# Performance work log

Measured on AMD Instinct MI355X. Metric: run time of the kernel, lower is better.

## Reference

```python
import jax, jax.numpy as jnp
import numpy as np

N = 50000      # nodes
E = 800000     # edges (before self-loops)
C_IN = 128
HID = 128
C_OUT = 64
B = 64         # graphs in batch
NEG_SLOPE = 0.2
EPS = 1e-16


def setup_inputs() -> dict:
    key = jax.random.key(0)
    ks = jax.random.split(key, 12)
    x = jax.random.normal(ks[0], (N, C_IN), dtype=jnp.float32)
    edge_index = jax.random.randint(ks[1], (2, E), 0, N, dtype=jnp.int64)
    batch = jnp.sort(jax.random.randint(ks[2], (N,), 0, B, dtype=jnp.int64))
    g1 = 1.0 / np.sqrt(C_IN)
    g2 = 1.0 / np.sqrt(HID)
    return {
        'x': x,
        'edge_index': edge_index,
        'batch': batch,
        'W1': jax.random.normal(ks[3], (C_IN, HID), jnp.float32) * g1,
        'a_src1': jax.random.normal(ks[4], (HID,), jnp.float32) * g2,
        'a_dst1': jax.random.normal(ks[5], (HID,), jnp.float32) * g2,
        'b1': jnp.zeros((HID,), jnp.float32),
        'W2': jax.random.normal(ks[6], (HID, C_OUT), jnp.float32) * g2,
        'a_src2': jax.random.normal(ks[7], (C_OUT,), jnp.float32) / np.sqrt(C_OUT),
        'a_dst2': jax.random.normal(ks[8], (C_OUT,), jnp.float32) / np.sqrt(C_OUT),
        'b2': jnp.zeros((C_OUT,), jnp.float32),
    }


def _gat_conv(x, src, dst, W, a_src, a_dst, b):
    # PyG GATConv, heads=1, self-loops already appended to (src, dst).
    h = x @ W                                   # [N, F]
    alpha = h[src] @ a_src + h[dst] @ a_dst     # [E'] per-edge logit
    alpha = jax.nn.leaky_relu(alpha, NEG_SLOPE)
    # segment softmax over incoming edges of each destination node
    amax = jax.ops.segment_max(alpha, dst, num_segments=N)
    e = jnp.exp(alpha - amax[dst])
    denom = jax.ops.segment_sum(e, dst, num_segments=N)
    att = e / (denom[dst] + EPS)                # [E']
    out = jax.ops.segment_sum(att[:, None] * h[src], dst, num_segments=N)
    return out + b


def reference(x, edge_index, batch, W1, a_src1, a_dst1, b1, W2, a_src2, a_dst2, b2):
    loop = jnp.arange(N, dtype=edge_index.dtype)
    src = jnp.concatenate([edge_index[0], loop])  # add_self_loops=True
    dst = jnp.concatenate([edge_index[1], loop])
    h = _gat_conv(x, src, dst, W1, a_src1, a_dst1, b1)
    h = jax.nn.relu(h)
    h = _gat_conv(h, src, dst, W2, a_src2, a_dst2, b2)
    # global mean pool over graph ids
    sums = jax.ops.segment_sum(h, batch, num_segments=B)          # [B, C_OUT]
    cnt = jax.ops.segment_sum(jnp.ones((N,), h.dtype), batch, num_segments=B)
    pooled = sums / jnp.maximum(cnt, 1.0)[:, None]
    return jax.nn.log_softmax(pooled, axis=1)
```

## Files before the change

kernel.cpp:

```cpp
#include <hip/hip_runtime.h>
#include <math.h>

#define NN 50000
#define EE 800000
#define EP (EE + NN)
#define COUT 64
#define BB 64
#define NEG_SLOPE 0.2f
#define EPSF 1e-16f
#define NPART 8
#define PNODES (NN / NPART)
#define CAPE 128
#define GM 782

typedef unsigned short u16;
typedef __attribute__((ext_vector_type(8))) short bf16x8;
typedef __attribute__((ext_vector_type(4))) float f32x4;

__device__ __forceinline__ u16 f2b(float f) {
    union { float f; unsigned u; } v; v.f = f;
    unsigned u = v.u;
    return (u16)((u + 0x7FFFu + ((u >> 16) & 1u)) >> 16);
}
__device__ __forceinline__ float b2f(u16 h) {
    union { unsigned u; float f; } v; v.u = ((unsigned)h) << 16;
    return v.f;
}
__device__ __forceinline__ float leaky(float v) {
    return (v > 0.f) ? v : NEG_SLOPE * v;
}

__global__ __launch_bounds__(256) void k_pre(const float* __restrict__ W1,
                                             const float* __restrict__ W2,
                                             u16* __restrict__ W1t,
                                             u16* __restrict__ W2t,
                                             int* __restrict__ deg,
                                             float* __restrict__ sums) {
    int b = blockIdx.x;
    if (b < 96) {
        int t = b * 256 + threadIdx.x;
        if (t < 128 * 128) {
            int c = t >> 7, k = t & 127;
            W1t[t] = f2b(W1[k * 128 + c]);
        } else {
            int o = t - 128 * 128;
            int c = o >> 7, k = o & 127;
            W2t[o] = f2b(W2[k * 64 + c]);
        }
    } else {
        int n = (b - 96) * 256 + threadIdx.x;
        if (n < NN) deg[n] = 0;
        if (n < BB * COUT) sums[n] = 0.f;
    }
}

__global__ __launch_bounds__(256) void k_scatter(const int* __restrict__ src,
                                                 const int* __restrict__ dst,
                                                 int* __restrict__ deg,
                                                 int* __restrict__ col_ell) {
    int v = blockIdx.x & (NPART - 1);
    int cid = blockIdx.x >> 3;
    int nchunk = gridDim.x >> 3;
    int lo = v * PNODES, hi = lo + PNODES;
    for (int e = cid * 256 + threadIdx.x; e < EP; e += nchunk * 256) {
        int dd = (e < EE) ? dst[e] : (e - EE);
        if (dd >= lo && dd < hi) {
            int s = (e < EE) ? src[e] : dd;
            int pos = atomicAdd(&deg[dd], 1);
            if (pos < CAPE) col_ell[(size_t)dd * CAPE + pos] = s;
        }
    }
}

template <int F, bool ABF16>
__device__ __forceinline__ void gemm_body(int bx,
                                          const void* __restrict__ Xv,
                                          const u16* __restrict__ Wt,
                                          u16* __restrict__ H,
                                          const float* __restrict__ a_src,
                                          const float* __restrict__ a_dst,
                                          float* __restrict__ sdot,
                                          float* __restrict__ ddot) {
    __shared__ u16 Ab[64 * 128];
    __shared__ u16 Bb[F * 128];
    int tid = threadIdx.x;
    int row0 = bx * 64;

    if (ABF16) {
        const u16* X = (const u16*)Xv;
        #pragma unroll
        for (int it = 0; it < 4; it++) {
            int c = it * 256 + tid;
            int row = c >> 4;
            int k8 = (c & 15) * 8;
            int grow = row0 + row;
            uint4 val = {0u, 0u, 0u, 0u};
            if (grow < NN) val = *(const uint4*)&X[(size_t)grow * 128 + k8];
            *(uint4*)&Ab[row * 128 + (k8 ^ ((row & 7) << 3))] = val;
        }
    } else {
        const float* X = (const float*)Xv;
        #pragma unroll
        for (int it = 0; it < 8; it++) {
            int c = it * 256 + tid;
            int e = c * 4;
            int row = e >> 7;
            int col = e & 127;
            int grow = row0 + row;
            float4 v = {0.f, 0.f, 0.f, 0.f};
            if (grow < NN) v = *(const float4*)&X[(size_t)grow * 128 + col];
            ushort4 o;
            o.x = f2b(v.x); o.y = f2b(v.y); o.z = f2b(v.z); o.w = f2b(v.w);
            *(ushort4*)&Ab[row * 128 + (col ^ ((row & 7) << 3))] = o;
        }
    }
    const int NB = F * 128 / 8 / 256;
    #pragma unroll
    for (int it = 0; it < NB; it++) {
        int c = it * 256 + tid;
        int col = c >> 4;
        int k8 = (c & 15) * 8;
        uint4 val = *(const uint4*)&Wt[col * 128 + k8];
        *(uint4*)&Bb[col * 128 + (k8 ^ ((col & 7) << 3))] = val;
    }
    __syncthreads();

    int w = tid >> 6, l = tid & 63;
    int g = l >> 4;
    int rA = l & 15;
    const int NT = F / 16;
    f32x4 acc[NT];
    #pragma unroll
    for (int ct = 0; ct < NT; ct++) {
        acc[ct][0] = 0.f; acc[ct][1] = 0.f; acc[ct][2] = 0.f; acc[ct][3] = 0.f;
    }
    int arow = w * 16 + rA;
    int abase = arow * 128;
    int sw = (rA & 7) << 3;
    #pragma unroll
    for (int ks = 0; ks < 4; ks++) {
        int koff = ks * 32 + g * 8;
        bf16x8 af = *(const bf16x8*)&Ab[abase + (koff ^ sw)];
        #pragma unroll
        for (int ct = 0; ct < NT; ct++) {
            int bcol = ct * 16 + rA;
            bf16x8 bfv = *(const bf16x8*)&Bb[bcol * 128 + (koff ^ sw)];
            acc[ct] = __builtin_amdgcn_mfma_f32_16x16x32_bf16(af, bfv, acc[ct], 0, 0, 0);
        }
    }

    float asv[NT], adv[NT];
    #pragma unroll
    for (int ct = 0; ct < NT; ct++) {
        asv[ct] = a_src[ct * 16 + rA];
        adv[ct] = a_dst[ct * 16 + rA];
    }
    float ps[4] = {0.f, 0.f, 0.f, 0.f};
    float pd[4] = {0.f, 0.f, 0.f, 0.f};
    #pragma unroll
    for (int ct = 0; ct < NT; ct++) {
        #pragma unroll
        for (int r = 0; r < 4; r++) {
            ps[r] += acc[ct][r] * asv[ct];
            pd[r] += acc[ct][r] * adv[ct];
        }
    }
    #pragma unroll
    for (int r = 0; r < 4; r++) {
        int grow = row0 + w * 16 + g * 4 + r;
        if (grow < NN) {
            #pragma unroll
            for (int ct = 0; ct < NT; ct++) {
                H[(size_t)grow * F + ct * 16 + rA] = f2b(acc[ct][r]);
            }
        }
    }
    #pragma unroll
    for (int r = 0; r < 4; r++) {
        #pragma unroll
        for (int off = 1; off < 16; off <<= 1) {
            ps[r] += __shfl_xor(ps[r], off);
            pd[r] += __shfl_xor(pd[r], off);
        }
    }
    if (rA == 0) {
        #pragma unroll
        for (int r = 0; r < 4; r++) {
            int grow = row0 + w * 16 + g * 4 + r;
            if (grow < NN) { sdot[grow] = ps[r]; ddot[grow] = pd[r]; }
        }
    }
}

__global__ __launch_bounds__(256) void k_gemm1(const float* __restrict__ x,
                                               const u16* __restrict__ W1t,
                                               u16* __restrict__ h1,
                                               const float* __restrict__ as1,
                                               const float* __restrict__ ad1,
                                               float* __restrict__ s1,
                                               float* __restrict__ d1) {
    gemm_body<128, false>(blockIdx.x, x, W1t, h1, as1, ad1, s1, d1);
}

__global__ __launch_bounds__(256) void k_gemm2(const u16* __restrict__ x2,
                                               const u16* __restrict__ W2t,
                                               u16* __restrict__ h2,
                                               const float* __restrict__ as2,
                                               const float* __restrict__ ad2,
                                               float* __restrict__ s2,
                                               float* __restrict__ d2) {
    gemm_body<64, true>(blockIdx.x, x2, W2t, h2, as2, ad2, s2, d2);
}

template <int ROWB>
__device__ __forceinline__ float stage_weights(const int* __restrict__ colrow,
                                               const float* __restrict__ s,
                                               float dn, int deg, int lane,
                                               float* __restrict__ wl,
                                               int* __restrict__ wc) {
    float M = -INFINITY;
    for (int e0 = 0; e0 < deg; e0 += 64) {
        int e = e0 + lane;
        float l = -INFINITY; int c = 0;
        if (e < deg) { c = colrow[e]; l = leaky(s[c] + dn); }
        wl[e0 + lane] = l;
        wc[e0 + lane] = c * ROWB;
        float cm = l;
        #pragma unroll
        for (int off = 32; off; off >>= 1) cm = fmaxf(cm, __shfl_xor(cm, off));
        M = fmaxf(M, cm);
    }
    float Sl = 0.f;
    for (int i0 = 0; i0 < deg; i0 += 64) {
        float u = __expf(wl[i0 + lane] - M);
        wl[i0 + lane] = u;
        Sl += u;
    }
    #pragma unroll
    for (int off = 32; off; off >>= 1) Sl += __shfl_xor(Sl, off);
    return 1.f / (Sl + EPSF);
}

__global__ __launch_bounds__(256) void k_fused1(const int* __restrict__ degv,
                                                const int* __restrict__ col_ell,
                                                const float* __restrict__ s,
                                                const float* __restrict__ d,
                                                const u16* __restrict__ H,
                                                const float* __restrict__ bias,
                                                u16* __restrict__ outb) {
    const int F = 128;
    __shared__ float wl[4][CAPE];
    __shared__ int   wc[4][CAPE];
    int w = threadIdx.x >> 6;
    int lane = threadIdx.x & 63;
    int n = blockIdx.x * 4 + w;
    int deg = degv[n];
    if (deg > CAPE) deg = CAPE;
    const int* colrow = col_ell + (size_t)n * CAPE;
    float dn = d[n];
    const char* Hb = (const char*)H + lane * 4;
    float2 acc = {0.f, 0.f};

    float invS = stage_weights<F * 2>(colrow, s, dn, deg, lane, wl[w], wc[w]);
    int i = 0;
    for (; i + 8 <= deg; i += 8) {
        float u0 = wl[w][i+0], u1 = wl[w][i+1], u2 = wl[w][i+2], u3 = wl[w][i+3];
        float u4 = wl[w][i+4], u5 = wl[w][i+5], u6 = wl[w][i+6], u7 = wl[w][i+7];
        int o0 = wc[w][i+0], o1 = wc[w][i+1], o2 = wc[w][i+2], o3 = wc[w][i+3];
        int o4 = wc[w][i+4], o5 = wc[w][i+5], o6 = wc[w][i+6], o7 = wc[w][i+7];
        ushort2 r0 = *(const ushort2*)(Hb + o0);
        ushort2 r1 = *(const ushort2*)(Hb + o1);
        ushort2 r2 = *(const ushort2*)(Hb + o2);
        ushort2 r3 = *(const ushort2*)(Hb + o3);
        ushort2 r4 = *(const ushort2*)(Hb + o4);
        ushort2 r5 = *(const ushort2*)(Hb + o5);
        ushort2 r6 = *(const ushort2*)(Hb + o6);
        ushort2 r7 = *(const ushort2*)(Hb + o7);
        acc.x += u0 * b2f(r0.x); acc.y += u0 * b2f(r0.y);
        acc.x += u1 * b2f(r1.x); acc.y += u1 * b2f(r1.y);
        acc.x += u2 * b2f(r2.x); acc.y += u2 * b2f(r2.y);
        acc.x += u3 * b2f(r3.x); acc.y += u3 * b2f(r3.y);
        acc.x += u4 * b2f(r4.x); acc.y += u4 * b2f(r4.y);
        acc.x += u5 * b2f(r5.x); acc.y += u5 * b2f(r5.y);
        acc.x += u6 * b2f(r6.x); acc.y += u6 * b2f(r6.y);
        acc.x += u7 * b2f(r7.x); acc.y += u7 * b2f(r7.y);
    }
    for (; i < deg; ++i) {
        float u = wl[w][i];
        ushort2 r = *(const ushort2*)(Hb + wc[w][i]);
        acc.x += u * b2f(r.x); acc.y += u * b2f(r.y);
    }
    float2 b = *(const float2*)&bias[lane * 2];
    acc.x = fmaxf(acc.x * invS + b.x, 0.f);
    acc.y = fmaxf(acc.y * invS + b.y, 0.f);
    ushort2 o; o.x = f2b(acc.x); o.y = f2b(acc.y);
    *(ushort2*)&outb[(size_t)n * F + lane * 2] = o;
}

#define NPW 4
__global__ __launch_bounds__(256) void k_fused2(const int* __restrict__ degv,
                                                const int* __restrict__ col_ell,
                                                const float* __restrict__ s,
                                                const float* __restrict__ d,
                                                const u16* __restrict__ H,
                                                const float* __restrict__ bias,
                                                const int* __restrict__ batch,
                                                float* __restrict__ sums) {
    const int F = 64;
    __shared__ float wl[4][CAPE];
    __shared__ int   wc[4][CAPE];
    int wave = threadIdx.x >> 6;
    int lane = threadIdx.x & 63;
    int base = (blockIdx.x * 4 + wave) * NPW;
    int lim = base + NPW;
    float bs = bias[lane];
    const char* Hb = (const char*)H + lane * 2;
    float gacc = 0.f;
    int gb = batch[base];

    for (int n = base; n < lim; ++n) {
        int b = batch[n];
        if (b != gb) {
            atomicAdd(&sums[gb * COUT + lane], gacc);
            gacc = 0.f; gb = b;
        }
        int deg = degv[n];
        if (deg > CAPE) deg = CAPE;
        const int* colrow = col_ell + (size_t)n * CAPE;
        float dn = d[n];
        float acc = 0.f;

        float invS = stage_weights<F * 2>(colrow, s, dn, deg, lane, wl[wave], wc[wave]);
        int i = 0;
        for (; i + 8 <= deg; i += 8) {
            float u0 = wl[wave][i+0], u1 = wl[wave][i+1], u2 = wl[wave][i+2], u3 = wl[wave][i+3];
            float u4 = wl[wave][i+4], u5 = wl[wave][i+5], u6 = wl[wave][i+6], u7 = wl[wave][i+7];
            int o0 = wc[wave][i+0], o1 = wc[wave][i+1], o2 = wc[wave][i+2], o3 = wc[wave][i+3];
            int o4 = wc[wave][i+4], o5 = wc[wave][i+5], o6 = wc[wave][i+6], o7 = wc[wave][i+7];
            u16 r0 = *(const u16*)(Hb + o0); u16 r1 = *(const u16*)(Hb + o1);
            u16 r2 = *(const u16*)(Hb + o2); u16 r3 = *(const u16*)(Hb + o3);
            u16 r4 = *(const u16*)(Hb + o4); u16 r5 = *(const u16*)(Hb + o5);
            u16 r6 = *(const u16*)(Hb + o6); u16 r7 = *(const u16*)(Hb + o7);
            acc += u0 * b2f(r0) + u1 * b2f(r1) + u2 * b2f(r2) + u3 * b2f(r3);
            acc += u4 * b2f(r4) + u5 * b2f(r5) + u6 * b2f(r6) + u7 * b2f(r7);
        }
        for (; i < deg; ++i) {
            acc += wl[wave][i] * b2f(*(const u16*)(Hb + wc[wave][i]));
        }
        gacc += acc * invS + bs;
    }
    atomicAdd(&sums[gb * COUT + lane], gacc);
}

__global__ __launch_bounds__(256) void k_logsm(const float* __restrict__ sums,
                                               const int* __restrict__ batch,
                                               float* __restrict__ out) {
    int wave = threadIdx.x >> 6;
    int lane = threadIdx.x & 63;
    int g = blockIdx.x * 4 + wave;
    if (g >= BB) return;
    int lo = 0, hi = NN;
    while (lo < hi) { int mid = (lo + hi) >> 1; if (batch[mid] < g) lo = mid + 1; else hi = mid; }
    int l2 = lo, h2 = NN;
    while (l2 < h2) { int mid = (l2 + h2) >> 1; if (batch[mid] < g + 1) l2 = mid + 1; else h2 = mid; }
    float cnt = (float)(h2 - lo);
    float mean = sums[g * COUT + lane] / fmaxf(cnt, 1.f);
    float mx = mean;
    #pragma unroll
    for (int off = 32; off; off >>= 1) mx = fmaxf(mx, __shfl_xor(mx, off));
    float ex = __expf(mean - mx);
    float sm = ex;
    #pragma unroll
    for (int off = 32; off; off >>= 1) sm += __shfl_xor(sm, off);
    out[g * COUT + lane] = mean - mx - logf(sm);
}

extern "C" void kernel_launch(void* const* d_in, const int* in_sizes, int n_in,
                              void* d_out, int out_size, void* d_ws, size_t ws_size,
                              hipStream_t stream) {
    const float* x      = (const float*)d_in[0];
    const int*   eidx   = (const int*)d_in[1];
    const int*   batch  = (const int*)d_in[2];
    const float* W1     = (const float*)d_in[3];
    const float* a_src1 = (const float*)d_in[4];
    const float* a_dst1 = (const float*)d_in[5];
    const float* b1     = (const float*)d_in[6];
    const float* W2     = (const float*)d_in[7];
    const float* a_src2 = (const float*)d_in[8];
    const float* a_dst2 = (const float*)d_in[9];
    const float* b2     = (const float*)d_in[10];
    float* out = (float*)d_out;

    const int* src = eidx;
    const int* dst = eidx + EE;

    char* w = (char*)d_ws;
    auto alloc = [&](size_t bytes) { void* p = (void*)w; w += (bytes + 255) & ~(size_t)255; return p; };
    float* sums  = (float*)alloc((size_t)BB * COUT * 4);
    float* s1    = (float*)alloc((size_t)NN * 4);
    float* d1    = (float*)alloc((size_t)NN * 4);
    float* s2    = (float*)alloc((size_t)NN * 4);
    float* d2    = (float*)alloc((size_t)NN * 4);
    int* deg     = (int*)alloc((size_t)NN * 4);
    int* col_ell = (int*)alloc((size_t)NN * CAPE * 4);
    u16* h1      = (u16*)alloc((size_t)NN * 128 * 2);
    u16* x2      = (u16*)alloc((size_t)NN * 128 * 2);
    u16* h2      = (u16*)alloc((size_t)NN * 64 * 2);
    u16* W1t     = (u16*)alloc((size_t)128 * 128 * 2);
    u16* W2t     = (u16*)alloc((size_t)64 * 128 * 2);

    dim3 blk(256);
    int gN4 = (NN + 3) / 4;

    k_pre<<<292, blk, 0, stream>>>(W1, W2, W1t, W2t, deg, sums);
    k_scatter<<<2048, blk, 0, stream>>>(src, dst, deg, col_ell);

    k_gemm1<<<GM, blk, 0, stream>>>(x, W1t, h1, a_src1, a_dst1, s1, d1);
    k_fused1<<<gN4, blk, 0, stream>>>(deg, col_ell, s1, d1, h1, b1, x2);

    k_gemm2<<<GM, blk, 0, stream>>>(x2, W2t, h2, a_src2, a_dst2, s2, d2);
    k_fused2<<<NN / (4 * NPW), blk, 0, stream>>>(deg, col_ell, s2, d2, h2, b2, batch, sums);

    k_logsm<<<(BB + 3) / 4, blk, 0, stream>>>(sums, batch, out);
}
```

Before: 151.0 us.

## Vectorize neighbor gathers across lane groups and vectorize edge scatter loads

Both aggregation kernels now split each wave into four lane groups, each handling a different neighbor. Each lane loads 16 bytes (layer 1) or 8 bytes (layer 2) of bf16 features per neighbor instead of 2 or 4 bytes, and partial sums are combined with cross-group shuffles. The edge scatter kernel reads destination indices as int4 and handles self-loops in a separate loop, which removes the per-edge branch. The aggregation loop rounds the degree up to a multiple of 8, so it relies on the staged weight and offset arrays holding zero weights and valid offsets in the padded slots. It also adds shuffle-reduction work and leaves only one lane group doing the writes.

```diff
diff --git a/kernel.cpp b/kernel.cpp
--- a/kernel.cpp
+++ b/kernel.cpp
@@ -25,6 +25,12 @@
 __device__ __forceinline__ float b2f(u16 h) {
     union { unsigned u; float f; } v; v.u = ((unsigned)h) << 16;
     return v.f;
+}
+__device__ __forceinline__ float lo16(unsigned v) {
+    union { unsigned u; float f; } x; x.u = v << 16; return x.f;
+}
+__device__ __forceinline__ float hi16(unsigned v) {
+    union { unsigned u; float f; } x; x.u = v & 0xffff0000u; return x.f;
 }
 __device__ __forceinline__ float leaky(float v) {
     return (v > 0.f) ? v : NEG_SLOPE * v;
@@ -62,13 +68,29 @@
     int cid = blockIdx.x >> 3;
     int nchunk = gridDim.x >> 3;
     int lo = v * PNODES, hi = lo + PNODES;
-    for (int e = cid * 256 + threadIdx.x; e < EP; e += nchunk * 256) {
-        int dd = (e < EE) ? dst[e] : (e - EE);
-        if (dd >= lo && dd < hi) {
-            int s = (e < EE) ? src[e] : dd;
-            int pos = atomicAdd(&deg[dd], 1);
-            if (pos < CAPE) col_ell[(size_t)dd * CAPE + pos] = s;
-        }
+    for (int q = cid * 256 + threadIdx.x; q < EE / 4; q += nchunk * 256) {
+        int4 d4 = *(const int4*)&dst[q * 4];
+        int e = q * 4;
+        if (d4.x >= lo && d4.x < hi) {
+            int pos = atomicAdd(&deg[d4.x], 1);
+            if (pos < CAPE) col_ell[(size_t)d4.x * CAPE + pos] = src[e];
+        }
+        if (d4.y >= lo && d4.y < hi) {
+            int pos = atomicAdd(&deg[d4.y], 1);
+            if (pos < CAPE) col_ell[(size_t)d4.y * CAPE + pos] = src[e + 1];
+        }
+        if (d4.z >= lo && d4.z < hi) {
+            int pos = atomicAdd(&deg[d4.z], 1);
+            if (pos < CAPE) col_ell[(size_t)d4.z * CAPE + pos] = src[e + 2];
+        }
+        if (d4.w >= lo && d4.w < hi) {
+            int pos = atomicAdd(&deg[d4.w], 1);
+            if (pos < CAPE) col_ell[(size_t)d4.w * CAPE + pos] = src[e + 3];
+        }
+    }
+    for (int n = lo + cid * 256 + threadIdx.x; n < hi; n += nchunk * 256) {
+        int pos = atomicAdd(&deg[n], 1);
+        if (pos < CAPE) col_ell[(size_t)n * CAPE + pos] = n;
     }
 }
 
@@ -258,43 +280,44 @@
     if (deg > CAPE) deg = CAPE;
     const int* colrow = col_ell + (size_t)n * CAPE;
     float dn = d[n];
-    const char* Hb = (const char*)H + lane * 4;
-    float2 acc = {0.f, 0.f};
 
     float invS = stage_weights<F * 2>(colrow, s, dn, deg, lane, wl[w], wc[w]);
-    int i = 0;
-    for (; i + 8 <= deg; i += 8) {
-        float u0 = wl[w][i+0], u1 = wl[w][i+1], u2 = wl[w][i+2], u3 = wl[w][i+3];
-        float u4 = wl[w][i+4], u5 = wl[w][i+5], u6 = wl[w][i+6], u7 = wl[w][i+7];
-        int o0 = wc[w][i+0], o1 = wc[w][i+1], o2 = wc[w][i+2], o3 = wc[w][i+3];
-        int o4 = wc[w][i+4], o5 = wc[w][i+5], o6 = wc[w][i+6], o7 = wc[w][i+7];
-        ushort2 r0 = *(const ushort2*)(Hb + o0);
-        ushort2 r1 = *(const ushort2*)(Hb + o1);
-        ushort2 r2 = *(const ushort2*)(Hb + o2);
-        ushort2 r3 = *(const ushort2*)(Hb + o3);
-        ushort2 r4 = *(const ushort2*)(Hb + o4);
-        ushort2 r5 = *(const ushort2*)(Hb + o5);
-        ushort2 r6 = *(const ushort2*)(Hb + o6);
-        ushort2 r7 = *(const ushort2*)(Hb + o7);
-        acc.x += u0 * b2f(r0.x); acc.y += u0 * b2f(r0.y);
-        acc.x += u1 * b2f(r1.x); acc.y += u1 * b2f(r1.y);
-        acc.x += u2 * b2f(r2.x); acc.y += u2 * b2f(r2.y);
-        acc.x += u3 * b2f(r3.x); acc.y += u3 * b2f(r3.y);
-        acc.x += u4 * b2f(r4.x); acc.y += u4 * b2f(r4.y);
-        acc.x += u5 * b2f(r5.x); acc.y += u5 * b2f(r5.y);
-        acc.x += u6 * b2f(r6.x); acc.y += u6 * b2f(r6.y);
-        acc.x += u7 * b2f(r7.x); acc.y += u7 * b2f(r7.y);
-    }
-    for (; i < deg; ++i) {
-        float u = wl[w][i];
-        ushort2 r = *(const ushort2*)(Hb + wc[w][i]);
-        acc.x += u * b2f(r.x); acc.y += u * b2f(r.y);
-    }
-    float2 b = *(const float2*)&bias[lane * 2];
-    acc.x = fmaxf(acc.x * invS + b.x, 0.f);
-    acc.y = fmaxf(acc.y * invS + b.y, 0.f);
-    ushort2 o; o.x = f2b(acc.x); o.y = f2b(acc.y);
-    *(ushort2*)&outb[(size_t)n * F + lane * 2] = o;
+
+    int g = lane >> 4;
+    int sub = lane & 15;
+    const char* Hb = (const char*)H + sub * 16;
+    float acc[8] = {0.f, 0.f, 0.f, 0.f, 0.f, 0.f, 0.f, 0.f};
+    int degR = (deg + 7) & ~7;
+    for (int i = 0; i < degR; i += 8) {
+        float u0 = wl[w][i + g];
+        int   o0 = wc[w][i + g];
+        float u1 = wl[w][i + 4 + g];
+        int   o1 = wc[w][i + 4 + g];
+        uint4 p0 = *(const uint4*)(Hb + o0);
+        uint4 p1 = *(const uint4*)(Hb + o1);
+        acc[0] += u0 * lo16(p0.x); acc[1] += u0 * hi16(p0.x);
+        acc[2] += u0 * lo16(p0.y); acc[3] += u0 * hi16(p0.y);
+        acc[4] += u0 * lo16(p0.z); acc[5] += u0 * hi16(p0.z);
+        acc[6] += u0 * lo16(p0.w); acc[7] += u0 * hi16(p0.w);
+        acc[0] += u1 * lo16(p1.x); acc[1] += u1 * hi16(p1.x);
+        acc[2] += u1 * lo16(p1.y); acc[3] += u1 * hi16(p1.y);
+        acc[4] += u1 * lo16(p1.z); acc[5] += u1 * hi16(p1.z);
+        acc[6] += u1 * lo16(p1.w); acc[7] += u1 * hi16(p1.w);
+    }
+    #pragma unroll
+    for (int j = 0; j < 8; j++) {
+        acc[j] += __shfl_xor(acc[j], 16);
+        acc[j] += __shfl_xor(acc[j], 32);
+    }
+    if (g == 0) {
+        ushort o8[8];
+        #pragma unroll
+        for (int j = 0; j < 8; j++) {
+            float v = fmaxf(acc[j] * invS + bias[sub * 8 + j], 0.f);
+            o8[j] = f2b(v);
+        }
+        *(uint4*)&outb[(size_t)n * F + sub * 8] = *(const uint4*)o8;
+    }
 }
 
 #define NPW 4
@@ -311,45 +334,62 @@
     __shared__ int   wc[4][CAPE];
     int wave = threadIdx.x >> 6;
     int lane = threadIdx.x & 63;
+    int g = lane >> 4;
+    int sub = lane & 15;
     int base = (blockIdx.x * 4 + wave) * NPW;
     int lim = base + NPW;
-    float bs = bias[lane];
-    const char* Hb = (const char*)H + lane * 2;
-    float gacc = 0.f;
+    float bs[4];
+    #pragma unroll
+    for (int j = 0; j < 4; j++) bs[j] = bias[sub * 4 + j];
+    const char* Hb = (const char*)H + sub * 8;
+    float gacc[4] = {0.f, 0.f, 0.f, 0.f};
     int gb = batch[base];
 
     for (int n = base; n < lim; ++n) {
         int b = batch[n];
         if (b != gb) {
-            atomicAdd(&sums[gb * COUT + lane], gacc);
-            gacc = 0.f; gb = b;
+            if (g == 0) {
+                #pragma unroll
+                for (int j = 0; j < 4; j++)
+                    atomicAdd(&sums[gb * COUT + sub * 4 + j], gacc[j]);
+            }
+            #pragma unroll
+            for (int j = 0; j < 4; j++) gacc[j] = 0.f;
+            gb = b;
         }
         int deg = degv[n];
         if (deg > CAPE) deg = CAPE;
         const int* colrow = col_ell + (size_t)n * CAPE;
         float dn = d[n];
-        float acc = 0.f;
 
         float invS = stage_weights<F * 2>(colrow, s, dn, deg, lane, wl[wave], wc[wave]);
-        int i = 0;
-        for (; i + 8 <= deg; i += 8) {
-            float u0 = wl[wave][i+0], u1 = wl[wave][i+1], u2 = wl[wave][i+2], u3 = wl[wave][i+3];
-            float u4 = wl[wave][i+4], u5 = wl[wave][i+5], u6 = wl[wave][i+6], u7 = wl[wave][i+7];
-            int o0 = wc[wave][i+0], o1 = wc[wave][i+1], o2 = wc[wave][i+2], o3 = wc[wave][i+3];
-            int o4 = wc[wave][i+4], o5 = wc[wave][i+5], o6 = wc[wave][i+6], o7 = wc[wave][i+7];
-            u16 r0 = *(const u16*)(Hb + o0); u16 r1 = *(const u16*)(Hb + o1);
-            u16 r2 = *(const u16*)(Hb + o2); u16 r3 = *(const u16*)(Hb + o3);
-            u16 r4 = *(const u16*)(Hb + o4); u16 r5 = *(const u16*)(Hb + o5);
-            u16 r6 = *(const u16*)(Hb + o6); u16 r7 = *(const u16*)(Hb + o7);
-            acc += u0 * b2f(r0) + u1 * b2f(r1) + u2 * b2f(r2) + u3 * b2f(r3);
-            acc += u4 * b2f(r4) + u5 * b2f(r5) + u6 * b2f(r6) + u7 * b2f(r7);
-        }
-        for (; i < deg; ++i) {
-            acc += wl[wave][i] * b2f(*(const u16*)(Hb + wc[wave][i]));
-        }
-        gacc += acc * invS + bs;
-    }
-    atomicAdd(&sums[gb * COUT + lane], gacc);
+
+        float acc[4] = {0.f, 0.f, 0.f, 0.f};
+        int degR = (deg + 7) & ~7;
+        for (int i = 0; i < degR; i += 8) {
+            float u0 = wl[wave][i + g];
+            int   o0 = wc[wave][i + g];
+            float u1 = wl[wave][i + 4 + g];
+            int   o1 = wc[wave][i + 4 + g];
+            uint2 p0 = *(const uint2*)(Hb + o0);
+            uint2 p1 = *(const uint2*)(Hb + o1);
+            acc[0] += u0 * lo16(p0.x); acc[1] += u0 * hi16(p0.x);
+            acc[2] += u0 * lo16(p0.y); acc[3] += u0 * hi16(p0.y);
+            acc[0] += u1 * lo16(p1.x); acc[1] += u1 * hi16(p1.x);
+            acc[2] += u1 * lo16(p1.y); acc[3] += u1 * hi16(p1.y);
+        }
+        #pragma unroll
+        for (int j = 0; j < 4; j++) {
+            acc[j] += __shfl_xor(acc[j], 16);
+            acc[j] += __shfl_xor(acc[j], 32);
+            gacc[j] += acc[j] * invS + bs[j];
+        }
+    }
+    if (g == 0) {
+        #pragma unroll
+        for (int j = 0; j < 4; j++)
+            atomicAdd(&sums[gb * COUT + sub * 4 + j], gacc[j]);
+    }
 }
 
 __global__ __launch_bounds__(256) void k_logsm(const float* __restrict__ sums,
```

Measured after the change: 182.8 us. 21.1% more time.
